# Kernel optimization log

Measured on AMD Instinct MI355X. Metric: run time of the kernel, lower is better.

Reference implementation:

```python
import jax, jax.numpy as jnp
import numpy as np

IMAGE_W = 256
IMAGE_H = 256
SIGMA = 0.2
EPS = 1e-07


def _gauss_filter(g, size, psize, pad):
    """g: [B,N] center coords in pixels. Returns [B,N,size,psize]."""
    # grid coords over padded canvas: value i - pad at row i (matches np.indices - pad)
    coords = jnp.arange(size + 2 * pad, dtype=jnp.float32) - pad          # [size+2pad]
    offs = jnp.arange(1, psize + 1, dtype=jnp.float32) - psize / 2 - 0.5  # [psize]
    mu = g[:, :, None] + offs[None, None, :]                              # [B,N,psize]
    F = jnp.exp(-(coords[None, None, :, None] - mu[:, :, None, :]) ** 2 / (2 * SIGMA ** 2))
    F = F / (F.sum(axis=2, keepdims=True) + EPS)
    return F[:, :, pad:size + pad]                                        # [B,N,size,psize]


def setup_inputs() -> dict:
    key = jax.random.key(0)
    k1, k2 = jax.random.split(key)
    brushes = jax.random.uniform(k1, (32, 64, 2), dtype=jnp.float32)
    patches = jax.random.normal(k2, (32, 64, 3, 16, 16), dtype=jnp.float32)
    return {"brushes": brushes, "patches": patches}


def reference(brushes, patches):
    B, N, C, ph, pw = patches.shape
    pad = ph // 2  # pad='half_patch'
    gx = brushes[:, :, 0] * IMAGE_W  # [B,N]
    gy = brushes[:, :, 1] * IMAGE_H
    Fx = _gauss_filter(gx, IMAGE_W, pw, pad)  # [B,N,w,pw]
    Fy = _gauss_filter(gy, IMAGE_H, ph, pad)  # [B,N,h,ph]
    # contract over pw: [B,N,C,w,ph]
    t = jnp.einsum('bnwq,bncpq->bncwp', Fx, patches)
    # contract over ph: [B,N,C,w,h]
    out = jnp.einsum('bncwp,bnhp->bncwh', t, Fy)
    out = out.mean(axis=1)            # [B,C,w,h]
    out = jnp.swapaxes(out, 2, 3)     # [B,C,h,w]
    return out
```

## Files before the change

kernel.cpp:

```cpp
#include <hip/hip_runtime.h>
#include <hip/hip_bf16.h>


#define TILE 16

__global__ __launch_bounds__(256) void brush_tile(
        const float* __restrict__ brushes,
        const float* __restrict__ patches,
        float* __restrict__ out)
{
    const int b   = blockIdx.z;
    const int tx  = blockIdx.x * TILE;
    const int ty  = blockIdx.y * TILE;
    const int tid = threadIdx.x;
    const int qi  = tid & 15;
    const int pi  = tid >> 4;
    const int w   = tx + qi;
    const int h   = ty + pi;

    __shared__ float  gxy[128];
    __shared__ unsigned long long smask;
    __shared__ float  invZ[32];
    __shared__ float4 T4[16 * 21];

    if (tid < 80)
        T4[(tid / 5) * 21 + 16 + (tid % 5)] = make_float4(0, 0, 0, 0);

    if (tid < 64) {
        float2 g = ((const float2*)brushes)[(b << 6) + tid];
        g.x *= 256.0f; g.y *= 256.0f;
        ((float2*)gxy)[tid] = g;
        const bool hit =
            (g.x >= (float)tx - 9.5f) & (g.x <= (float)tx + 24.5f) &
            (g.y >= (float)ty - 9.5f) & (g.y <= (float)ty + 24.5f);
        const unsigned long long m = __ballot(hit);
        if (tid == 0) smask = m;
    }
    __syncthreads();
    unsigned long long mask = smask;

    float acc0 = 0.0f, acc1 = 0.0f, acc2 = 0.0f;
    const float E25 = 1.3887944e-11f;

    while (mask) {
        const int n = __builtin_ctzll(mask);
        mask &= mask - 1;
        const float gx = gxy[2 * n], gy = gxy[2 * n + 1];

        const float* pb = patches + (size_t)((b << 6) + n) * 768;
        const float r0 = pb[tid];
        const float r1 = pb[tid + 256];
        const float r2 = pb[tid + 512];

        if (tid < 32) {
            const int axis = tid >> 4, q = tid & 15;
            const float g  = axis ? gy : gx;
            const float mu = g + (float)q - 7.5f;
            const float fl = floorf(mu);
            float Z = 0.0f;
#pragma unroll
            for (int d = -1; d <= 2; ++d) {
                const float c = fl + (float)d;
                if (c >= -8.0f && c <= 263.0f) {
                    const float u = c - mu;
                    Z += __expf(-12.5f * u * u);
                }
            }
            invZ[tid] = 1.0f / (Z + 1e-7f);
        }
        __syncthreads();

        const float zx = invZ[qi];
        const float v0 = r0 * zx, v1 = r1 * zx, v2 = r2 * zx;

        {
            const float ax  = (float)w - gx + 7.5f;
            const bool  okx = (ax >= -2.5f) & (ax <= 17.5f);
            int qlo = (int)ceilf(ax - 2.0f);
            qlo = qlo < 0 ? 0 : (qlo > 15 ? 15 : qlo);
            float d0 = ax - (float)qlo;
            d0 = fminf(fmaxf(d0, -3.0f), 3.0f);
            float wgt = okx ? __expf(-12.5f * d0 * d0) : 0.0f;
            float u   = __expf(25.0f * d0 - 12.5f);
            const int base = ((pi & 3) << 4) + qlo;
            float4 s = make_float4(0, 0, 0, 0);
#pragma unroll
            for (int j = 0; j < 5; ++j) {
                const float a0 = __shfl(v0, base + j, 64);
                const float a1 = __shfl(v1, base + j, 64);
                const float a2 = __shfl(v2, base + j, 64);
                const float wj = (qlo + j < 16) ? wgt : 0.0f;
                s.x += wj * a0; s.y += wj * a1; s.z += wj * a2;
                wgt *= u; u *= E25;
            }
            const float zy = invZ[16 + pi];
            s.x *= zy; s.y *= zy; s.z *= zy;
            T4[qi * 21 + pi] = s;
        }
        __syncthreads();

        {
            const float ay = (float)h - gy + 7.5f;
            if (ay >= -2.5f && ay <= 17.5f) {
                int plo = (int)ceilf(ay - 2.0f);
                plo = plo < 0 ? 0 : (plo > 15 ? 15 : plo);
                const float d0 = ay - (float)plo;
                float wgt = __expf(-12.5f * d0 * d0);
                float u   = __expf(25.0f * d0 - 12.5f);
                const float4* row = &T4[qi * 21 + plo];
#pragma unroll
                for (int j = 0; j < 5; ++j) {
                    const float4 v = row[j];
                    acc0 += wgt * v.x; acc1 += wgt * v.y; acc2 += wgt * v.z;
                    wgt *= u; u *= E25;
                }
            }
        }
    }

    const float sc = 1.0f / 64.0f;
    float* ob = out + (((size_t)(b * 3)) << 16) + (h << 8) + w;
    ob[0]       = acc0 * sc;
    ob[1 << 16] = acc1 * sc;
    ob[2 << 16] = acc2 * sc;
}

extern "C" void kernel_launch(void* const* d_in, const int* in_sizes, int n_in,
                              void* d_out, int out_size, void* d_ws, size_t ws_size,
                              hipStream_t stream) {
    const float* brushes = (const float*)d_in[0];
    const float* patches = (const float*)d_in[1];
    float* out = (float*)d_out;
    brush_tile<<<dim3(16, 16, 32), dim3(256), 0, stream>>>(brushes, patches, out);
}
```

Measured before the change: 78.55 us.

## Enlarge output tile to 32x32 per block with double-buffered LDS and shuffles

Each block now covers a 32x32 output tile instead of 16x16, with each thread accumulating four pixels, so patch loads and the normalisation factors are reused across more output. Brush coordinates and inverse normalisers are passed through wave shuffles rather than shared memory, and the intermediate buffer is double-buffered, which removes two barriers per brush. The trade-off is fewer blocks (2048 instead of 8192), more brushes intersecting each tile, and more registers per thread.

New measurement: 80.64 us. 2.7% more time.

```diff
diff --git a/kernel.cpp b/kernel.cpp
--- a/kernel.cpp
+++ b/kernel.cpp
@@ -2,60 +2,60 @@
 #include <hip/hip_bf16.h>
 
 
-#define TILE 16
+#define E25 1.3887944e-11f
 
-__global__ __launch_bounds__(256) void brush_tile(
+__global__ __launch_bounds__(256) void brush_tile32(
         const float* __restrict__ brushes,
         const float* __restrict__ patches,
         float* __restrict__ out)
 {
-    const int b   = blockIdx.z;
-    const int tx  = blockIdx.x * TILE;
-    const int ty  = blockIdx.y * TILE;
-    const int tid = threadIdx.x;
-    const int qi  = tid & 15;
-    const int pi  = tid >> 4;
-    const int w   = tx + qi;
-    const int h   = ty + pi;
+    const int b    = blockIdx.z;
+    const int tx   = blockIdx.x << 5;
+    const int ty   = blockIdx.y << 5;
+    const int tid  = threadIdx.x;
+    const int lane = tid & 63;
+    const int qi   = tid & 15;
+    const int pi   = tid >> 4;
 
-    __shared__ float  gxy[128];
-    __shared__ unsigned long long smask;
-    __shared__ float  invZ[32];
-    __shared__ float4 T4[16 * 21];
+    __shared__ float4 T4[2 * 32 * 21];
 
-    if (tid < 80)
-        T4[(tid / 5) * 21 + 16 + (tid % 5)] = make_float4(0, 0, 0, 0);
+    for (int i = tid; i < 320; i += 256) {
+        const int buf = i / 160, r = i % 160;
+        T4[buf * 672 + (r / 5) * 21 + 16 + (r % 5)] = make_float4(0, 0, 0, 0);
+    }
 
-    if (tid < 64) {
-        float2 g = ((const float2*)brushes)[(b << 6) + tid];
-        g.x *= 256.0f; g.y *= 256.0f;
-        ((float2*)gxy)[tid] = g;
-        const bool hit =
-            (g.x >= (float)tx - 9.5f) & (g.x <= (float)tx + 24.5f) &
-            (g.y >= (float)ty - 9.5f) & (g.y <= (float)ty + 24.5f);
-        const unsigned long long m = __ballot(hit);
-        if (tid == 0) smask = m;
-    }
-    __syncthreads();
-    unsigned long long mask = smask;
+    const float2 g0 = ((const float2*)brushes)[(b << 6) + lane];
+    const float bx = g0.x * 256.0f, by = g0.y * 256.0f;
+    const bool hit =
+        (bx >= (float)tx - 9.5f) & (bx <= (float)tx + 40.5f) &
+        (by >= (float)ty - 9.5f) & (by <= (float)ty + 40.5f);
+    unsigned long long mask = __ballot(hit);
 
-    float acc0 = 0.0f, acc1 = 0.0f, acc2 = 0.0f;
-    const float E25 = 1.3887944e-11f;
+    float acc[2][2][3];
+#pragma unroll
+    for (int a = 0; a < 2; ++a)
+#pragma unroll
+        for (int h2 = 0; h2 < 2; ++h2)
+            acc[a][h2][0] = acc[a][h2][1] = acc[a][h2][2] = 0.0f;
 
+    int it = 0;
     while (mask) {
         const int n = __builtin_ctzll(mask);
         mask &= mask - 1;
-        const float gx = gxy[2 * n], gy = gxy[2 * n + 1];
+        const float gx = __shfl(bx, n, 64);
+        const float gy = __shfl(by, n, 64);
+        const int buf = (it & 1) * 672; ++it;
 
         const float* pb = patches + (size_t)((b << 6) + n) * 768;
         const float r0 = pb[tid];
         const float r1 = pb[tid + 256];
         const float r2 = pb[tid + 512];
 
-        if (tid < 32) {
-            const int axis = tid >> 4, q = tid & 15;
-            const float g  = axis ? gy : gx;
-            const float mu = g + (float)q - 7.5f;
+        float invz;
+        {
+            const int k = lane & 31;
+            const float g  = (k >> 4) ? gy : gx;
+            const float mu = g + (float)(k & 15) - 7.5f;
             const float fl = floorf(mu);
             float Z = 0.0f;
 #pragma unroll
@@ -66,16 +66,22 @@
                     Z += __expf(-12.5f * u * u);
                 }
             }
-            invZ[tid] = 1.0f / (Z + 1e-7f);
+            invz = 1.0f / (Z + 1e-7f);
         }
-        __syncthreads();
-
-        const float zx = invZ[qi];
+        const float zx  = __shfl(invz, qi, 64);
+        const float zyp = __shfl(invz, 16 + pi, 64);
         const float v0 = r0 * zx, v1 = r1 * zx, v2 = r2 * zx;
 
-        {
-            const float ax  = (float)w - gx + 7.5f;
-            const bool  okx = (ax >= -2.5f) & (ax <= 17.5f);
+        const bool doA = (gx <= (float)tx + 24.5f);
+        const bool doB = (gx >= (float)tx + 6.5f);
+
+        float4 sA = make_float4(0, 0, 0, 0), sB = sA;
+#pragma unroll
+        for (int half = 0; half < 2; ++half) {
+            const bool go = half ? doB : doA;
+            if (!go) continue;
+            const float ax = (float)(tx + (half << 4) + qi) - gx + 7.5f;
+            const bool okx = (ax >= -2.5f) & (ax <= 17.5f);
             int qlo = (int)ceilf(ax - 2.0f);
             qlo = qlo < 0 ? 0 : (qlo > 15 ? 15 : qlo);
             float d0 = ax - (float)qlo;
@@ -93,36 +99,52 @@
                 s.x += wj * a0; s.y += wj * a1; s.z += wj * a2;
                 wgt *= u; u *= E25;
             }
-            const float zy = invZ[16 + pi];
-            s.x *= zy; s.y *= zy; s.z *= zy;
-            T4[qi * 21 + pi] = s;
+            s.x *= zyp; s.y *= zyp; s.z *= zyp;
+            if (half) sB = s; else sA = s;
         }
+        T4[buf + qi * 21 + pi]        = sA;
+        T4[buf + (qi + 16) * 21 + pi] = sB;
         __syncthreads();
 
-        {
-            const float ay = (float)h - gy + 7.5f;
-            if (ay >= -2.5f && ay <= 17.5f) {
-                int plo = (int)ceilf(ay - 2.0f);
-                plo = plo < 0 ? 0 : (plo > 15 ? 15 : plo);
-                const float d0 = ay - (float)plo;
-                float wgt = __expf(-12.5f * d0 * d0);
-                float u   = __expf(25.0f * d0 - 12.5f);
-                const float4* row = &T4[qi * 21 + plo];
+#pragma unroll
+        for (int h2 = 0; h2 < 2; ++h2) {
+            const float ay = (float)(ty + (h2 << 4) + pi) - gy + 7.5f;
+            if (ay < -2.5f || ay > 17.5f) continue;
+            int plo = (int)ceilf(ay - 2.0f);
+            plo = plo < 0 ? 0 : (plo > 15 ? 15 : plo);
+            const float d0 = ay - (float)plo;
+            float wy[5];
+            float wgt = __expf(-12.5f * d0 * d0);
+            float u   = __expf(25.0f * d0 - 12.5f);
+#pragma unroll
+            for (int j = 0; j < 5; ++j) { wy[j] = wgt; wgt *= u; u *= E25; }
+#pragma unroll
+            for (int a = 0; a < 2; ++a) {
+                if (!(a ? doB : doA)) continue;
+                const float4* row = &T4[buf + (qi + (a << 4)) * 21 + plo];
+                float s0 = 0.0f, s1 = 0.0f, s2 = 0.0f;
 #pragma unroll
                 for (int j = 0; j < 5; ++j) {
                     const float4 v = row[j];
-                    acc0 += wgt * v.x; acc1 += wgt * v.y; acc2 += wgt * v.z;
-                    wgt *= u; u *= E25;
+                    s0 += wy[j] * v.x; s1 += wy[j] * v.y; s2 += wy[j] * v.z;
                 }
+                acc[a][h2][0] += s0; acc[a][h2][1] += s1; acc[a][h2][2] += s2;
             }
         }
     }
 
     const float sc = 1.0f / 64.0f;
-    float* ob = out + (((size_t)(b * 3)) << 16) + (h << 8) + w;
-    ob[0]       = acc0 * sc;
-    ob[1 << 16] = acc1 * sc;
-    ob[2 << 16] = acc2 * sc;
+#pragma unroll
+    for (int a = 0; a < 2; ++a)
+#pragma unroll
+        for (int h2 = 0; h2 < 2; ++h2) {
+            const int w = tx + (a << 4) + qi;
+            const int h = ty + (h2 << 4) + pi;
+            float* ob = out + (((size_t)(b * 3)) << 16) + (h << 8) + w;
+            ob[0]       = acc[a][h2][0] * sc;
+            ob[1 << 16] = acc[a][h2][1] * sc;
+            ob[2 << 16] = acc[a][h2][2] * sc;
+        }
 }
 
 extern "C" void kernel_launch(void* const* d_in, const int* in_sizes, int n_in,
@@ -131,5 +153,5 @@
     const float* brushes = (const float*)d_in[0];
     const float* patches = (const float*)d_in[1];
     float* out = (float*)d_out;
-    brush_tile<<<dim3(16, 16, 32), dim3(256), 0, stream>>>(brushes, patches, out);
+    brush_tile32<<<dim3(8, 8, 32), dim3(256), 0, stream>>>(brushes, patches, out);
 }
```

## Prescale patches in prep kernel and double-buffer brush loop with prefetch

Applied to the files above, without the earlier changes.

A new prep kernel multiplies each patch by its x and y normalisation factors once and writes the result to workspace, so the tile kernel no longer computes invZ for every brush in every tile. The tile kernel now computes the hit mask in registers with ballot instead of through shared memory, prefetches the next brush's patch while processing the current one, and double-buffers the T4 shared array. This removes two of the three barriers per brush. It adds a second launch and a workspace write and read of the full patch tensor.

Measured after the change: 81.55 us. 1.04x slower.

```diff
diff --git a/kernel.cpp b/kernel.cpp
--- a/kernel.cpp
+++ b/kernel.cpp
@@ -2,119 +2,141 @@
 #include <hip/hip_bf16.h>
 
 
-#define TILE 16
+#define E25 1.3887944e-11f
+
+__global__ __launch_bounds__(256) void brush_prep(
+        const float* __restrict__ brushes,
+        const float* __restrict__ patches,
+        float* __restrict__ patchP)
+{
+    const int bn   = blockIdx.x;
+    const int tid  = threadIdx.x;
+    const int lane = tid & 63;
+    const int qi   = tid & 15;
+    const int pi   = tid >> 4;
+
+    const float2 g = ((const float2*)brushes)[bn];
+    const float gx = g.x * 256.0f, gy = g.y * 256.0f;
+
+    const int k = lane & 31;
+    const float gg = (k >> 4) ? gy : gx;
+    const float mu = gg + (float)(k & 15) - 7.5f;
+    const float fl = floorf(mu);
+    float Z = 0.0f;
+#pragma unroll
+    for (int d = -1; d <= 2; ++d) {
+        const float c = fl + (float)d;
+        if (c >= -8.0f && c <= 263.0f) {
+            const float u = c - mu;
+            Z += __expf(-12.5f * u * u);
+        }
+    }
+    const float invz = 1.0f / (Z + 1e-7f);
+    const float s = __shfl(invz, qi, 64) * __shfl(invz, 16 + pi, 64);
+
+    const float* pb = patches + (size_t)bn * 768;
+    float*       wp = patchP  + (size_t)bn * 768;
+    wp[tid]       = pb[tid]       * s;
+    wp[tid + 256] = pb[tid + 256] * s;
+    wp[tid + 512] = pb[tid + 512] * s;
+}
 
 __global__ __launch_bounds__(256) void brush_tile(
         const float* __restrict__ brushes,
-        const float* __restrict__ patches,
+        const float* __restrict__ patchP,
         float* __restrict__ out)
 {
-    const int b   = blockIdx.z;
-    const int tx  = blockIdx.x * TILE;
-    const int ty  = blockIdx.y * TILE;
-    const int tid = threadIdx.x;
-    const int qi  = tid & 15;
-    const int pi  = tid >> 4;
-    const int w   = tx + qi;
-    const int h   = ty + pi;
+    const int b    = blockIdx.z;
+    const int tx   = blockIdx.x << 4;
+    const int ty   = blockIdx.y << 4;
+    const int tid  = threadIdx.x;
+    const int lane = tid & 63;
+    const int qi   = tid & 15;
+    const int pi   = tid >> 4;
+    const int w    = tx + qi;
+    const int h    = ty + pi;
 
-    __shared__ float  gxy[128];
-    __shared__ unsigned long long smask;
-    __shared__ float  invZ[32];
-    __shared__ float4 T4[16 * 21];
+    __shared__ float4 T4[2 * 16 * 21];
 
-    if (tid < 80)
-        T4[(tid / 5) * 21 + 16 + (tid % 5)] = make_float4(0, 0, 0, 0);
+    if (tid < 160) {
+        const int buf = tid / 80, r = tid % 80;
+        T4[buf * 336 + (r / 5) * 21 + 16 + (r % 5)] = make_float4(0, 0, 0, 0);
+    }
 
-    if (tid < 64) {
-        float2 g = ((const float2*)brushes)[(b << 6) + tid];
-        g.x *= 256.0f; g.y *= 256.0f;
-        ((float2*)gxy)[tid] = g;
-        const bool hit =
-            (g.x >= (float)tx - 9.5f) & (g.x <= (float)tx + 24.5f) &
-            (g.y >= (float)ty - 9.5f) & (g.y <= (float)ty + 24.5f);
-        const unsigned long long m = __ballot(hit);
-        if (tid == 0) smask = m;
-    }
-    __syncthreads();
-    unsigned long long mask = smask;
+    const float2 g0 = ((const float2*)brushes)[(b << 6) + lane];
+    const float bx = g0.x * 256.0f, by = g0.y * 256.0f;
+    const bool hit =
+        (bx >= (float)tx - 9.5f) & (bx <= (float)tx + 24.5f) &
+        (by >= (float)ty - 9.5f) & (by <= (float)ty + 24.5f);
+    unsigned long long mask = __ballot(hit);
 
     float acc0 = 0.0f, acc1 = 0.0f, acc2 = 0.0f;
-    const float E25 = 1.3887944e-11f;
 
-    while (mask) {
-        const int n = __builtin_ctzll(mask);
+    if (mask) {
+        int n = __builtin_ctzll(mask);
         mask &= mask - 1;
-        const float gx = gxy[2 * n], gy = gxy[2 * n + 1];
+        const float* wp = patchP + (size_t)((b << 6) + n) * 768;
+        float a0 = wp[tid], a1 = wp[tid + 256], a2 = wp[tid + 512];
+        int it = 0;
 
-        const float* pb = patches + (size_t)((b << 6) + n) * 768;
-        const float r0 = pb[tid];
-        const float r1 = pb[tid + 256];
-        const float r2 = pb[tid + 512];
+        while (true) {
+            int nn = -1;
+            float p0, p1, p2;
+            if (mask) {
+                nn = __builtin_ctzll(mask);
+                mask &= mask - 1;
+                const float* wq = patchP + (size_t)((b << 6) + nn) * 768;
+                p0 = wq[tid]; p1 = wq[tid + 256]; p2 = wq[tid + 512];
+            }
 
-        if (tid < 32) {
-            const int axis = tid >> 4, q = tid & 15;
-            const float g  = axis ? gy : gx;
-            const float mu = g + (float)q - 7.5f;
-            const float fl = floorf(mu);
-            float Z = 0.0f;
+            const float gx = __shfl(bx, n, 64);
+            const float gy = __shfl(by, n, 64);
+            const int buf = (it & 1) * 336;
+
+            {
+                const float ax  = (float)w - gx + 7.5f;
+                const bool  okx = (ax >= -2.5f) & (ax <= 17.5f);
+                int qlo = (int)ceilf(ax - 2.0f);
+                qlo = qlo < 0 ? 0 : (qlo > 15 ? 15 : qlo);
+                float d0 = ax - (float)qlo;
+                d0 = fminf(fmaxf(d0, -3.0f), 3.0f);
+                float wgt = okx ? __expf(-12.5f * d0 * d0) : 0.0f;
+                float u   = __expf(25.0f * d0 - 12.5f);
+                const int base = ((pi & 3) << 4) + qlo;
+                float4 s = make_float4(0, 0, 0, 0);
 #pragma unroll
-            for (int d = -1; d <= 2; ++d) {
-                const float c = fl + (float)d;
-                if (c >= -8.0f && c <= 263.0f) {
-                    const float u = c - mu;
-                    Z += __expf(-12.5f * u * u);
+                for (int j = 0; j < 5; ++j) {
+                    const float t0 = __shfl(a0, base + j, 64);
+                    const float t1 = __shfl(a1, base + j, 64);
+                    const float t2 = __shfl(a2, base + j, 64);
+                    const float wj = (qlo + j < 16) ? wgt : 0.0f;
+                    s.x += wj * t0; s.y += wj * t1; s.z += wj * t2;
+                    wgt *= u; u *= E25;
+                }
+                T4[buf + qi * 21 + pi] = s;
+            }
+            __syncthreads();
+
+            {
+                const float ay = (float)h - gy + 7.5f;
+                if (ay >= -2.5f && ay <= 17.5f) {
+                    int plo = (int)ceilf(ay - 2.0f);
+                    plo = plo < 0 ? 0 : (plo > 15 ? 15 : plo);
+                    const float d0 = ay - (float)plo;
+                    float wgt = __expf(-12.5f * d0 * d0);
+                    float u   = __expf(25.0f * d0 - 12.5f);
+                    const float4* row = &T4[buf + qi * 21 + plo];
+#pragma unroll
+                    for (int j = 0; j < 5; ++j) {
+                        const float4 v = row[j];
+                        acc0 += wgt * v.x; acc1 += wgt * v.y; acc2 += wgt * v.z;
+                        wgt *= u; u *= E25;
+                    }
                 }
             }
-            invZ[tid] = 1.0f / (Z + 1e-7f);
-        }
-        __syncthreads();
 
-        const float zx = invZ[qi];
-        const float v0 = r0 * zx, v1 = r1 * zx, v2 = r2 * zx;
-
-        {
-            const float ax  = (float)w - gx + 7.5f;
-            const bool  okx = (ax >= -2.5f) & (ax <= 17.5f);
-            int qlo = (int)ceilf(ax - 2.0f);
-            qlo = qlo < 0 ? 0 : (qlo > 15 ? 15 : qlo);
-            float d0 = ax - (float)qlo;
-            d0 = fminf(fmaxf(d0, -3.0f), 3.0f);
-            float wgt = okx ? __expf(-12.5f * d0 * d0) : 0.0f;
-            float u   = __expf(25.0f * d0 - 12.5f);
-            const int base = ((pi & 3) << 4) + qlo;
-            float4 s = make_float4(0, 0, 0, 0);
-#pragma unroll
-            for (int j = 0; j < 5; ++j) {
-                const float a0 = __shfl(v0, base + j, 64);
-                const float a1 = __shfl(v1, base + j, 64);
-                const float a2 = __shfl(v2, base + j, 64);
-                const float wj = (qlo + j < 16) ? wgt : 0.0f;
-                s.x += wj * a0; s.y += wj * a1; s.z += wj * a2;
-                wgt *= u; u *= E25;
-            }
-            const float zy = invZ[16 + pi];
-            s.x *= zy; s.y *= zy; s.z *= zy;
-            T4[qi * 21 + pi] = s;
-        }
-        __syncthreads();
-
-        {
-            const float ay = (float)h - gy + 7.5f;
-            if (ay >= -2.5f && ay <= 17.5f) {
-                int plo = (int)ceilf(ay - 2.0f);
-                plo = plo < 0 ? 0 : (plo > 15 ? 15 : plo);
-                const float d0 = ay - (float)plo;
-                float wgt = __expf(-12.5f * d0 * d0);
-                float u   = __expf(25.0f * d0 - 12.5f);
-                const float4* row = &T4[qi * 21 + plo];
-#pragma unroll
-                for (int j = 0; j < 5; ++j) {
-                    const float4 v = row[j];
-                    acc0 += wgt * v.x; acc1 += wgt * v.y; acc2 += wgt * v.z;
-                    wgt *= u; u *= E25;
-                }
-            }
+            if (nn < 0) break;
+            n = nn; a0 = p0; a1 = p1; a2 = p2; ++it;
         }
     }
 
@@ -130,6 +152,8 @@
                               hipStream_t stream) {
     const float* brushes = (const float*)d_in[0];
     const float* patches = (const float*)d_in[1];
-    float* out = (float*)d_out;
-    brush_tile<<<dim3(16, 16, 32), dim3(256), 0, stream>>>(brushes, patches, out);
+    float* out    = (float*)d_out;
+    float* patchP = (float*)d_ws;
+    brush_prep<<<dim3(32 * 64), dim3(256), 0, stream>>>(brushes, patches, patchP);
+    brush_tile<<<dim3(16, 16, 32), dim3(256), 0, stream>>>(brushes, patchP, out);
 }
```
